# Optimization experiments

Measured on AMD Instinct MI355X. Metric: run time of the kernel, lower is better.

## Reference

```python
import jax, jax.numpy as jnp
import numpy as np

P_DROP = 0.2
NEG_SLOPE = 0.2


def setup_inputs() -> dict:
    key = jax.random.key(0)
    ks = jax.random.split(key, 12)
    N, E = 50000, 800000
    IN, H1, H2, OUT = 256, 256, 128, 64
    x = jax.random.normal(ks[0], (N, IN), dtype=jnp.float32)
    adj_rows = jax.random.randint(ks[1], (E,), 0, N, dtype=jnp.int32)
    adj_cols = jax.random.randint(ks[2], (E,), 0, N, dtype=jnp.int32)
    adj_vals = jax.random.uniform(ks[3], (E,), dtype=jnp.float32)
    W1 = jax.random.normal(ks[4], (H1, IN), dtype=jnp.float32) * (1.0 / np.sqrt(IN))
    b1 = jax.random.normal(ks[5], (H1,), dtype=jnp.float32) * 0.01
    W2 = jax.random.normal(ks[6], (H2, H1), dtype=jnp.float32) * (1.0 / np.sqrt(H1))
    b2 = jax.random.normal(ks[7], (H2,), dtype=jnp.float32) * 0.01
    W3 = jax.random.normal(ks[8], (OUT, H2), dtype=jnp.float32) * (1.0 / np.sqrt(H2))
    b3 = jax.random.normal(ks[9], (OUT,), dtype=jnp.float32) * 0.01
    mask1 = jax.random.bernoulli(ks[10], 1.0 - P_DROP, (N, H1))
    mask2 = jax.random.bernoulli(ks[11], 1.0 - P_DROP, (N, H2))
    return {"x": x, "adj_rows": adj_rows, "adj_cols": adj_cols, "adj_vals": adj_vals,
            "W1": W1, "b1": b1, "W2": W2, "b2": b2, "W3": W3, "b3": b3,
            "mask1": mask1, "mask2": mask2}


def _spmm(rows, cols, vals, h, n_nodes):
    # sparse adjacency matmul: out[r] = sum_e vals[e] * h[cols[e]] for rows[e]==r
    msgs = vals[:, None] * h[cols]  # [E, d] irregular gather
    return jax.ops.segment_sum(msgs, rows, num_segments=n_nodes)


def _gcn_layer(x, W, b, rows, cols, vals, n_nodes):
    h = x @ W.T + b  # nn.Linear
    return _spmm(rows, cols, vals, h, n_nodes)


def reference(x, adj_rows, adj_cols, adj_vals, W1, b1, W2, b2, W3, b3, mask1, mask2):
    N = x.shape[0]
    keep = 1.0 / (1.0 - P_DROP)
    h = _gcn_layer(x, W1, b1, adj_rows, adj_cols, adj_vals, N)
    h = jnp.where(h >= 0, h, NEG_SLOPE * h)
    h = jnp.where(mask1, h * keep, 0.0)
    h = _gcn_layer(h, W2, b2, adj_rows, adj_cols, adj_vals, N)
    h = jnp.where(h >= 0, h, NEG_SLOPE * h)
    h = jnp.where(mask2, h * keep, 0.0)
    z = _gcn_layer(h, W3, b3, adj_rows, adj_cols, adj_vals, N)
    return z
```

## Files before the change

### kernel.cpp

```cpp
#include <hip/hip_runtime.h>


typedef unsigned short ushort_t;
typedef __attribute__((ext_vector_type(8))) short bf16x8;
typedef __attribute__((ext_vector_type(4))) float f32x4;
typedef __attribute__((ext_vector_type(2))) unsigned int u32x2;
typedef __attribute__((ext_vector_type(4))) unsigned int u32x4;

__device__ __forceinline__ float bf2f(ushort_t u) {
  return __uint_as_float(((unsigned int)u) << 16);
}
__device__ __forceinline__ ushort_t f2bf(float f) {
  unsigned int u = __float_as_uint(f);
  return (ushort_t)((u + 0x7FFFu + ((u >> 16) & 1u)) >> 16);
}
__device__ __forceinline__ float read_f(const void* p, int fm, size_t i) {
  return fm ? bf2f(((const ushort_t*)p)[i]) : ((const float*)p)[i];
}

__device__ __forceinline__ size_t frag_off(int m, int k, int K) {
  return (size_t)(m >> 4) * 16 * K + ((size_t)(k >> 5) << 9) +
         (((k >> 3) & 3) << 7) + ((m & 15) << 3) + (k & 7);
}

__device__ __forceinline__ bool mask_keep(const void* mask, int mm, size_t o) {
  switch (mm) {
    case 1:  return ((const int*)mask)[o] != 0;
    case 2:  return ((const unsigned int*)mask)[o] != 0u;
    case 3:  return ((const ushort_t*)mask)[o] != 0;
    default: return ((const unsigned char*)mask)[o] != 0;
  }
}

__global__ void prep_kernel(const void* __restrict__ x,
                            const void* __restrict__ m1,
                            const void* __restrict__ m2,
                            int* __restrict__ modes,
                            int* __restrict__ zero_region, int zn) {
  if (blockIdx.x == 0) {
    __shared__ int bfok;
    if (threadIdx.x == 0) bfok = 1;
    __syncthreads();
    for (int i = threadIdx.x; i < 8192; i += blockDim.x) {
      ushort_t h = ((const ushort_t*)x)[i];
      int e = (h >> 7) & 0xFF;
      if (!(h == 0 || (e >= 95 && e <= 133))) atomicAnd(&bfok, 0);
    }
    __syncthreads();
    if (threadIdx.x == 0) modes[0] = bfok;
  } else if (blockIdx.x <= 2) {
    const void* p = (blockIdx.x == 1) ? m1 : m2;
    __shared__ int ok[4];
    if (threadIdx.x < 4) ok[threadIdx.x] = 1;
    __syncthreads();
    for (int i = threadIdx.x; i < 4096; i += blockDim.x) {
      unsigned int w = ((const unsigned int*)p)[i];
      if (!(w == 0u || w == 1u)) atomicAnd(&ok[0], 0);
      if (!(w == 0u || w == 0x3F800000u)) atomicAnd(&ok[1], 0);
      unsigned int h16 = w >> 16, l16 = w & 0xFFFFu;
      if (!((h16 == 0u || h16 == 0x3F80u) && (l16 == 0u || l16 == 0x3F80u)))
        atomicAnd(&ok[2], 0);
      if (((w | (w >> 8) | (w >> 16) | (w >> 24)) & 0xFEu) != 0u) atomicAnd(&ok[3], 0);
    }
    __syncthreads();
    if (threadIdx.x == 0)
      modes[blockIdx.x] = ok[0] ? 1 : (ok[1] ? 2 : (ok[2] ? 3 : 0));
  } else {
    int i = (blockIdx.x - 3) * blockDim.x + threadIdx.x;
    int stride = (gridDim.x - 3) * blockDim.x;
    for (; i < zn; i += stride) zero_region[i] = 0;
  }
}

__global__ void hist_kernel(const int* __restrict__ rows, int* __restrict__ cnt, int E) {
  int i = blockIdx.x * blockDim.x + threadIdx.x;
  int stride = gridDim.x * blockDim.x;
  for (; i < E; i += stride) atomicAdd(&cnt[rows[i]], 1);
}

__global__ void scan_part_kernel(const int* __restrict__ cnt, int* __restrict__ part, int n) {
  __shared__ int s[256];
  int i = blockIdx.x * 256 + threadIdx.x;
  s[threadIdx.x] = (i < n) ? cnt[i] : 0;
  __syncthreads();
  for (int off = 128; off > 0; off >>= 1) {
    if (threadIdx.x < off) s[threadIdx.x] += s[threadIdx.x + off];
    __syncthreads();
  }
  if (threadIdx.x == 0) part[blockIdx.x] = s[0];
}

__global__ __launch_bounds__(1024) void scan_top_kernel(int* __restrict__ part, int P) {
  __shared__ int s[1024];
  int t = threadIdx.x;
  int v = (t < P) ? part[t] : 0;
  s[t] = v;
  __syncthreads();
  for (int off = 1; off < 1024; off <<= 1) {
    int x = s[t];
    int y = (t >= off) ? s[t - off] : 0;
    __syncthreads();
    s[t] = x + y;
    __syncthreads();
  }
  if (t < P) part[t] = s[t] - v;
}

__global__ void scan_apply_kernel(const int* __restrict__ cnt, const int* __restrict__ part,
                                  int* __restrict__ row_start, int n) {
  __shared__ int s[256];
  int base = part[blockIdx.x];
  int i = blockIdx.x * 256 + threadIdx.x;
  int v = (i < n) ? cnt[i] : 0;
  s[threadIdx.x] = v;
  __syncthreads();
  for (int off = 1; off < 256; off <<= 1) {
    int x = s[threadIdx.x];
    int y = (threadIdx.x >= off) ? s[threadIdx.x - off] : 0;
    __syncthreads();
    s[threadIdx.x] = x + y;
    __syncthreads();
  }
  if (i < n) row_start[i] = base + s[threadIdx.x] - v;
  if (i == n - 1) row_start[n] = base + s[threadIdx.x];
}

__global__ void scatter_convert_kernel(
    const int* __restrict__ rows, const int* __restrict__ cols,
    const void* __restrict__ vals, const int* __restrict__ fm_p,
    const int* __restrict__ row_start, int* __restrict__ fill,
    int* __restrict__ binfill, int2* __restrict__ bins, int cap, int use_bins,
    int2* __restrict__ ecv, int E,
    const void* __restrict__ W1, const void* __restrict__ W2, const void* __restrict__ W3,
    const void* __restrict__ b1, const void* __restrict__ b2, const void* __restrict__ b3,
    const void* __restrict__ x,
    ushort_t* __restrict__ whi, ushort_t* __restrict__ wlo,
    float* __restrict__ biasf, ushort_t* __restrict__ xbf,
    int n1, int n2, int n3, int h1, int h2, int h3, int K1, int K2, int K3,
    int nx) {
  int fm = *fm_p;
  const int BIN_BLOCKS = 512;
  if (blockIdx.x < BIN_BLOCKS) {
    if (use_bins) {
      __shared__ int hist[8];
      __shared__ int gbase[8];
      int tid = threadIdx.x;
      int xcd = blockIdx.x & 7;
      for (int tb = blockIdx.x; tb * 1024 < E; tb += BIN_BLOCKS) {
        int base = tb * 1024;
        if (tid < 8) hist[tid] = 0;
        __syncthreads();
        int rr[4], cc[4], pp[4], rk[4]; float vv[4];
#pragma unroll
        for (int j = 0; j < 4; ++j) {
          int i = base + j * 256 + tid;
          if (i < E) {
            rr[j] = rows[i]; cc[j] = cols[i]; vv[j] = read_f(vals, fm, i);
            pp[j] = rr[j] >> 13;
            rk[j] = atomicAdd(&hist[pp[j]], 1);
          } else {
            pp[j] = -1;
          }
        }
        __syncthreads();
        if (tid < 8)
          gbase[tid] = atomicAdd(&binfill[(xcd << 4) + tid], hist[tid]);
        __syncthreads();
#pragma unroll
        for (int j = 0; j < 4; ++j) {
          if (pp[j] >= 0) {
            int pos = gbase[pp[j]] + rk[j];
            if (pos < cap) {
              bins[(size_t)((xcd << 3) + pp[j]) * cap + pos] =
                  make_int2((rr[j] << 16) | cc[j], __float_as_int(vv[j]));
            } else {
              int pr = atomicAdd(&fill[rr[j]], 1);
              ecv[row_start[rr[j]] + pr] = make_int2(cc[j], __float_as_int(vv[j]));
            }
          }
        }
      }
    } else {
      int i = blockIdx.x * blockDim.x + threadIdx.x;
      int stride = BIN_BLOCKS * blockDim.x;
      for (; i < E; i += stride) {
        int r = rows[i];
        int pos = atomicAdd(&fill[r], 1);
        ecv[row_start[r] + pos] = make_int2(cols[i], __float_as_int(read_f(vals, fm, i)));
      }
    }
  } else {
    int wtot = n1 + n2 + n3;
    int btot = h1 + h2 + h3;
    int nx4 = (fm == 1) ? 0 : nx / 4;
    int total = wtot + btot + nx4;
    int i = (blockIdx.x - BIN_BLOCKS) * blockDim.x + threadIdx.x;
    int stride = (gridDim.x - BIN_BLOCKS) * blockDim.x;
    for (; i < total; i += stride) {
      if (i < wtot) {
        const void* src; int j, K; size_t base;
        if (i < n1) { src = W1; j = i; K = K1; base = 0; }
        else if (i < n1 + n2) { src = W2; j = i - n1; K = K2; base = n1; }
        else { src = W3; j = i - n1 - n2; K = K3; base = (size_t)n1 + n2; }
        int n = j / K, k = j - n * K;
        float v = read_f(src, fm, j);
        ushort_t h = f2bf(v);
        size_t o = base + frag_off(n, k, K);
        whi[o] = h;
        wlo[o] = f2bf(v - bf2f(h));
      } else if (i < wtot + btot) {
        int k = i - wtot;
        const void* src; int j;
        if (k < h1) { src = b1; j = k; }
        else if (k < h1 + h2) { src = b2; j = k - h1; }
        else { src = b3; j = k - h1 - h2; }
        biasf[k] = read_f(src, fm, j);
      } else {
        int k4 = i - wtot - btot;
        int m = k4 / (K1 / 4);
        int k0 = (k4 - m * (K1 / 4)) * 4;
        f32x4 v = ((const f32x4*)x)[k4];
        ushort_t p0 = f2bf(v[0]), p1 = f2bf(v[1]), p2 = f2bf(v[2]), p3 = f2bf(v[3]);
        size_t o = frag_off(m, k0, K1);
        *(u32x2*)(xbf + o) = (u32x2){
            (unsigned int)p0 | ((unsigned int)p1 << 16),
            (unsigned int)p2 | ((unsigned int)p3 << 16)};
      }
    }
  }
}

__global__ __launch_bounds__(256) void bin_scatter_kernel(
    const int2* __restrict__ bins, const int* __restrict__ binfill,
    const int* __restrict__ row_start, int* __restrict__ fill,
    int2* __restrict__ ecv, int cap) {
  int p = blockIdx.x & 7, q = blockIdx.x >> 3;
#pragma unroll 1
  for (int x = 0; x < 8; ++x) {
    int n = binfill[x * 16 + p];
    if (n > cap) n = cap;
    const int2* bp = bins + (size_t)((x << 3) + p) * cap;
    for (int e = q * 256 + (int)threadIdx.x; e < n; e += 128 * 256) {
      int2 ent = bp[e];
      int r = ((unsigned int)ent.x) >> 16;
      int c = ent.x & 0xFFFF;
      int pos = atomicAdd(&fill[r], 1);
      ecv[row_start[r] + pos] = make_int2(c, ent.y);
    }
  }
}

template<int KC>
__device__ __forceinline__ void load_afrag(const ushort_t* __restrict__ A,
                                           const ushort_t* __restrict__ Xrow,
                                           bool rowA, int mtile, int K,
                                           int lane, int mr, int quad, int M,
                                           bf16x8* dst) {
  if (rowA) {
    int rr = mtile * 16 + mr;
    if (rr >= M) rr = M - 1;
    const ushort_t* ap = Xrow + (size_t)rr * K + quad * 8;
#pragma unroll
    for (int kc = 0; kc < KC; ++kc) dst[kc] = *(const bf16x8*)(ap + kc * 32);
  } else {
    const ushort_t* ap = A + (size_t)mtile * 16 * K + lane * 8;
#pragma unroll
    for (int kc = 0; kc < KC; ++kc) dst[kc] = *(const bf16x8*)(ap + kc * 512);
  }
}

template<int KC>
__global__ __launch_bounds__(256) void gemm_breg_kernel(
    const ushort_t* __restrict__ A,
    const ushort_t* __restrict__ Xrow, const int* __restrict__ fm_p,
    const ushort_t* __restrict__ Whi, const ushort_t* __restrict__ Wlo,
    const float* __restrict__ bias, ushort_t* __restrict__ g, int ldg,
    int M, int nct) {
  const int K = KC * 32;
  int wave = threadIdx.x >> 6, lane = threadIdx.x & 63;
  int gw = blockIdx.x * 4 + wave;
  int NW = gridDim.x * 4;
  int mr = lane & 15, quad = lane >> 4;
  int ct = gw % nct;
  int nrt = (M + 15) >> 4;
  int ntasks = nct * nrt;
  if (gw >= ntasks) return;

  bool rowA = (Xrow != nullptr) && (*fm_p != 0);

  bf16x8 wh[KC], wl[KC];
  {
    const ushort_t* wp = Whi + (size_t)ct * 16 * K + lane * 8;
    const ushort_t* wq = Wlo + (size_t)ct * 16 * K + lane * 8;
#pragma unroll
    for (int kc = 0; kc < KC; ++kc) {
      wh[kc] = *(const bf16x8*)(wp + kc * 512);
      wl[kc] = *(const bf16x8*)(wq + kc * 512);
    }
  }
  int col = ct * 16 + mr;
  float bv = bias[col];

  int task = gw;
  bf16x8 af[KC];
  load_afrag<KC>(A, Xrow, rowA, task / nct, K, lane, mr, quad, M, af);

#pragma unroll 1
  for (;;) {
    int next = task + NW;
    bool has_next = next < ntasks;
    bf16x8 afn[KC];
    if (has_next)
      load_afrag<KC>(A, Xrow, rowA, next / nct, K, lane, mr, quad, M, afn);

    f32x4 acc[4];
#pragma unroll
    for (int t = 0; t < 4; ++t) acc[t] = (f32x4){0.f, 0.f, 0.f, 0.f};
#pragma unroll
    for (int kc = 0; kc < KC; ++kc) {
      acc[(2 * kc) & 3] = __builtin_amdgcn_mfma_f32_16x16x32_bf16(af[kc], wh[kc], acc[(2 * kc) & 3], 0, 0, 0);
      acc[(2 * kc + 1) & 3] = __builtin_amdgcn_mfma_f32_16x16x32_bf16(af[kc], wl[kc], acc[(2 * kc + 1) & 3], 0, 0, 0);
    }
    int m0 = (task / nct) * 16;
#pragma unroll
    for (int r = 0; r < 4; ++r) {
      int row = m0 + quad * 4 + r;
      float s = ((acc[0][r] + acc[1][r]) + (acc[2][r] + acc[3][r])) + bv;
      if (row < M) g[(size_t)row * ldg + col] = f2bf(s);
    }
    if (!has_next) break;
#pragma unroll
    for (int kc = 0; kc < KC; ++kc) af[kc] = afn[kc];
    task = next;
  }
}

template<int MODE, int VEC>
__global__ __launch_bounds__(256) void spmm8_kernel(
    const int* __restrict__ row_start, const int2* __restrict__ ecv,
    const ushort_t* __restrict__ G, int D,
    const void* __restrict__ mask, const int* __restrict__ mmode_p,
    void* __restrict__ outp, int N) {
  __shared__ ushort_t stage[1024];
  int wave = threadIdx.x >> 6, lane = threadIdx.x & 63;
  int r = blockIdx.x * 4 + wave;
  bool active = r < N;
  float a[VEC];
#pragma unroll
  for (int q = 0; q < VEC; ++q) a[q] = 0.f;
  int f0 = lane * VEC;

  if (active) {
    int e  = __builtin_amdgcn_readfirstlane(row_start[r]);
    int e1 = __builtin_amdgcn_readfirstlane(row_start[r + 1]);
    for (; e + 8 <= e1; e += 8) {
      int2 cv[8];
#pragma unroll
      for (int j = 0; j < 8; ++j) cv[j] = ecv[e + j];
      if (VEC == 4) {
        u32x2 gg[8];
#pragma unroll
        for (int j = 0; j < 8; ++j)
          gg[j] = *(const u32x2*)(G + (size_t)cv[j].x * D + f0);
#pragma unroll
        for (int j = 0; j < 8; ++j) {
          float v = __int_as_float(cv[j].y);
          a[0] += v * bf2f((ushort_t)gg[j][0]);
          a[1] += v * bf2f((ushort_t)(gg[j][0] >> 16));
          a[2] += v * bf2f((ushort_t)gg[j][1]);
          a[3] += v * bf2f((ushort_t)(gg[j][1] >> 16));
        }
      } else if (VEC == 2) {
        unsigned int gg[8];
#pragma unroll
        for (int j = 0; j < 8; ++j)
          gg[j] = *(const unsigned int*)(G + (size_t)cv[j].x * D + f0);
#pragma unroll
        for (int j = 0; j < 8; ++j) {
          float v = __int_as_float(cv[j].y);
          a[0] += v * bf2f((ushort_t)gg[j]);
          a[1] += v * bf2f((ushort_t)(gg[j] >> 16));
        }
      } else {
        ushort_t h[8];
#pragma unroll
        for (int j = 0; j < 8; ++j) h[j] = G[(size_t)cv[j].x * D + f0];
#pragma unroll
        for (int j = 0; j < 8; ++j) a[0] += __int_as_float(cv[j].y) * bf2f(h[j]);
      }
    }
    if (e < e1) {
      int idx[8]; float v[8];
#pragma unroll
      for (int j = 0; j < 8; ++j) {
        int ee = e + j;
        bool ok = ee < e1;
        int2 cv = ecv[ok ? ee : e1 - 1];
        idx[j] = cv.x;
        v[j] = ok ? __int_as_float(cv.y) : 0.f;
      }
      if (VEC == 4) {
        u32x2 gg[8];
#pragma unroll
        for (int j = 0; j < 8; ++j)
          gg[j] = *(const u32x2*)(G + (size_t)idx[j] * D + f0);
#pragma unroll
        for (int j = 0; j < 8; ++j) {
          a[0] += v[j] * bf2f((ushort_t)gg[j][0]);
          a[1] += v[j] * bf2f((ushort_t)(gg[j][0] >> 16));
          a[2] += v[j] * bf2f((ushort_t)gg[j][1]);
          a[3] += v[j] * bf2f((ushort_t)(gg[j][1] >> 16));
        }
      } else if (VEC == 2) {
        unsigned int gg[8];
#pragma unroll
        for (int j = 0; j < 8; ++j)
          gg[j] = *(const unsigned int*)(G + (size_t)idx[j] * D + f0);
#pragma unroll
        for (int j = 0; j < 8; ++j) {
          a[0] += v[j] * bf2f((ushort_t)gg[j]);
          a[1] += v[j] * bf2f((ushort_t)(gg[j] >> 16));
        }
      } else {
        ushort_t h[8];
#pragma unroll
        for (int j = 0; j < 8; ++j) h[j] = G[(size_t)idx[j] * D + f0];
#pragma unroll
        for (int j = 0; j < 8; ++j) a[0] += v[j] * bf2f(h[j]);
      }
    }
  }

  if (MODE == 1) {
    if (active) {
      size_t om = (size_t)r * D + f0;
      int mm = *mmode_p;
      bool keep[VEC];
      if (mm == 1 || mm == 2) {
        if (VEC == 4) {
          u32x4 mv = *(const u32x4*)((const unsigned int*)mask + om);
#pragma unroll
          for (int q = 0; q < VEC; ++q) keep[q] = mv[q] != 0u;
        } else if (VEC == 2) {
          u32x2 mv = *(const u32x2*)((const unsigned int*)mask + om);
#pragma unroll
          for (int q = 0; q < VEC; ++q) keep[q] = mv[q] != 0u;
        } else {
          keep[0] = ((const unsigned int*)mask)[om] != 0u;
        }
      } else if (mm == 3) {
        if (VEC == 4) {
          u32x2 mv = *(const u32x2*)((const ushort_t*)mask + om);
          keep[0] = (mv[0] & 0xFFFFu) != 0u; keep[1] = (mv[0] >> 16) != 0u;
          keep[2] = (mv[1] & 0xFFFFu) != 0u; keep[3] = (mv[1] >> 16) != 0u;
        } else if (VEC == 2) {
          unsigned int mv = *(const unsigned int*)((const ushort_t*)mask + om);
          keep[0] = (mv & 0xFFFFu) != 0u; keep[1] = (mv >> 16) != 0u;
        } else {
          keep[0] = ((const ushort_t*)mask)[om] != 0;
        }
      } else {
        if (VEC == 4) {
          unsigned int mv = *(const unsigned int*)((const unsigned char*)mask + om);
          keep[0] = (mv & 0xFFu) != 0u;        keep[1] = ((mv >> 8) & 0xFFu) != 0u;
          keep[2] = ((mv >> 16) & 0xFFu) != 0u; keep[3] = (mv >> 24) != 0u;
        } else if (VEC == 2) {
          unsigned int mv = *(const unsigned short*)((const unsigned char*)mask + om);
          keep[0] = (mv & 0xFFu) != 0u; keep[1] = ((mv >> 8) & 0xFFu) != 0u;
        } else {
          keep[0] = ((const unsigned char*)mask)[om] != 0;
        }
      }
#pragma unroll
      for (int q = 0; q < VEC; ++q) {
        float t = a[q];
        t = (t >= 0.f) ? t : 0.2f * t;
        t = keep[q] ? t * 1.25f : 0.f;
        stage[wave * D + f0 + q] = f2bf(t);
      }
    }
    __syncthreads();
    if (threadIdx.x < D) {
      int g = threadIdx.x >> 3, s = threadIdx.x & 7;
      int kc = g >> 2, quad = g & 3;
      int sr = s >> 1;
      int r0 = blockIdx.x * 4;
      if (r0 + sr < N) {
        int kk = kc * 32 + quad * 8 + (s & 1) * 4;
        size_t dst = (size_t)(r0 >> 4) * 16 * D + ((size_t)kc << 9) +
                     (quad << 7) + ((r0 & 15) << 3) + s * 4;
        *(u32x2*)((ushort_t*)outp + dst) = *(const u32x2*)(stage + sr * D + kk);
      }
    }
  } else {
    if (active) {
      size_t o = (size_t)r * D + f0;
#pragma unroll
      for (int q = 0; q < VEC; ++q) ((float*)outp)[o + q] = a[q];
    }
  }
}

extern "C" void kernel_launch(void* const* d_in, const int* in_sizes, int n_in,
                              void* d_out, int out_size, void* d_ws, size_t ws_size,
                              hipStream_t stream) {
  const void* x     = d_in[0];
  const int*  rows  = (const int*)d_in[1];
  const int*  cols  = (const int*)d_in[2];
  const void* vals  = d_in[3];
  const void* W1    = d_in[4];
  const void* b1    = d_in[5];
  const void* W2    = d_in[6];
  const void* b2    = d_in[7];
  const void* W3    = d_in[8];
  const void* b3    = d_in[9];
  const void* mask1 = d_in[10];
  const void* mask2 = d_in[11];

  const int H1  = in_sizes[5];
  const int H2  = in_sizes[7];
  const int OUT = in_sizes[9];
  const int IN  = in_sizes[4] / H1;
  const int N   = in_sizes[0] / IN;
  const int E   = in_sizes[1];
  const int W1n = in_sizes[4], W2n = in_sizes[6], W3n = in_sizes[8];
  const int Np  = ((N + 15) / 16) * 16;
  const int CAP = (E >> 5) + 2048;
  const int use_bins = (N <= 65535) ? 1 : 0;

  char* ws = (char*)d_ws;
  size_t off = 0;
  auto alloc = [&](size_t bytes) -> void* {
    void* p = ws + off;
    off = (off + bytes + 255) & ~(size_t)255;
    return p;
  };
  int*      modes     = (int*)alloc(4 * 4);
  int*      row_start = (int*)alloc((size_t)(N + 1) * 4);
  int*      cnt       = (int*)alloc((size_t)N * 8 + 512);
  int*      part      = (int*)alloc(1024 * 4);
  int2*     ecv       = (int2*)alloc((size_t)E * 8);
  int2*     bins      = (int2*)alloc((size_t)64 * CAP * 8);
  ushort_t* whi       = (ushort_t*)alloc((size_t)(W1n + W2n + W3n) * 2);
  ushort_t* wlo       = (ushort_t*)alloc((size_t)(W1n + W2n + W3n) * 2);
  float*    biasf     = (float*)alloc((size_t)(H1 + H2 + OUT) * 4);
  ushort_t* bufA      = (ushort_t*)alloc((size_t)Np * H1 * 2);
  ushort_t* bufB      = (ushort_t*)alloc((size_t)Np * H1 * 2);
  ushort_t* bufC      = (ushort_t*)alloc((size_t)Np * H1 * 2);

  int* fmode   = modes;
  int* mm1     = modes + 1;
  int* mm2     = modes + 2;
  int* fill    = cnt + N;
  int* binfill = cnt + 2 * N;
  ushort_t* w1hi = whi,             *w1lo = wlo;
  ushort_t* w2hi = whi + W1n,       *w2lo = wlo + W1n;
  ushort_t* w3hi = whi + W1n + W2n, *w3lo = wlo + W1n + W2n;

  prep_kernel<<<259, 256, 0, stream>>>(x, mask1, mask2, modes, cnt, 2 * N + 128);

  const int P = (N + 255) / 256;
  hist_kernel<<<1024, 256, 0, stream>>>(rows, cnt, E);
  scan_part_kernel<<<P, 256, 0, stream>>>(cnt, part, N);
  scan_top_kernel<<<1, 1024, 0, stream>>>(part, P);
  scan_apply_kernel<<<P, 256, 0, stream>>>(cnt, part, row_start, N);

  scatter_convert_kernel<<<2560, 256, 0, stream>>>(
      rows, cols, vals, fmode, row_start, fill, binfill, bins, CAP, use_bins,
      ecv, E, W1, W2, W3, b1, b2, b3, x, whi, wlo, biasf, bufA,
      W1n, W2n, W3n, H1, H2, OUT, IN, H1, H2, N * IN);
  if (use_bins) {
    bin_scatter_kernel<<<1024, 256, 0, stream>>>(
        bins, binfill, row_start, fill, ecv, CAP);
  }

  const int GEMM_BLOCKS = 1024;
  int spmm_grid = (N + 3) / 4;

  gemm_breg_kernel<8><<<GEMM_BLOCKS, 256, 0, stream>>>(
      bufA, (const ushort_t*)x, fmode, w1hi, w1lo, biasf, bufB, H1, N, H1 / 16);
  spmm8_kernel<1, 4><<<spmm_grid, 256, 0, stream>>>(
      row_start, ecv, bufB, H1, mask1, mm1, bufC, N);
  gemm_breg_kernel<8><<<GEMM_BLOCKS, 256, 0, stream>>>(
      bufC, nullptr, fmode, w2hi, w2lo, biasf + H1, bufB, H2, N, H2 / 16);
  spmm8_kernel<1, 2><<<spmm_grid, 256, 0, stream>>>(
      row_start, ecv, bufB, H2, mask2, mm2, bufA, N);
  gemm_breg_kernel<4><<<GEMM_BLOCKS, 256, 0, stream>>>(
      bufA, nullptr, fmode, w3hi, w3lo, biasf + H1 + H2, bufB, OUT, N, OUT / 16);
  spmm8_kernel<0, 1><<<spmm_grid, 256, 0, stream>>>(
      row_start, ecv, bufB, OUT, nullptr, fmode, d_out, N);
}
```

Baseline: 441.7 us.

## Restructure CSR build: fuse histogram into binning, overlap scatter with first GEMM

Weight and bias conversion moves into the prep kernel. The row histogram is fused into the binning pass, whose overflow entries now go to a separate buffer instead of being written to CSR directly. The final CSR scatter shares one launch with the layer-1 GEMM, which does not depend on the CSR. This removes two launches and a separate pass over the rows array, and lets the atomic-heavy scatter run alongside GEMM work. The cost is extra atomics on cnt inside the binning loop, a serialised overflow counter, and an extra E-sized workspace buffer.

Result: faster. 423.9 us (-4.0%).

```diff
diff --git a/kernel.cpp b/kernel.cpp
--- a/kernel.cpp
+++ b/kernel.cpp
@@ -23,20 +23,19 @@
          (((k >> 3) & 3) << 7) + ((m & 15) << 3) + (k & 7);
 }
 
-__device__ __forceinline__ bool mask_keep(const void* mask, int mm, size_t o) {
-  switch (mm) {
-    case 1:  return ((const int*)mask)[o] != 0;
-    case 2:  return ((const unsigned int*)mask)[o] != 0u;
-    case 3:  return ((const ushort_t*)mask)[o] != 0;
-    default: return ((const unsigned char*)mask)[o] != 0;
-  }
-}
-
 __global__ void prep_kernel(const void* __restrict__ x,
                             const void* __restrict__ m1,
                             const void* __restrict__ m2,
                             int* __restrict__ modes,
-                            int* __restrict__ zero_region, int zn) {
+                            int* __restrict__ zero_region, int zn,
+                            const void* __restrict__ W1, const void* __restrict__ W2,
+                            const void* __restrict__ W3,
+                            const void* __restrict__ b1, const void* __restrict__ b2,
+                            const void* __restrict__ b3,
+                            ushort_t* __restrict__ whi, ushort_t* __restrict__ wlo,
+                            float* __restrict__ biasf,
+                            int n1, int n2, int n3, int h1, int h2, int h3,
+                            int K1, int K2, int K3) {
   if (blockIdx.x == 0) {
     __shared__ int bfok;
     if (threadIdx.x == 0) bfok = 1;
@@ -65,17 +64,45 @@
     __syncthreads();
     if (threadIdx.x == 0)
       modes[blockIdx.x] = ok[0] ? 1 : (ok[1] ? 2 : (ok[2] ? 3 : 0));
+  } else if (blockIdx.x < 35) {
+    __shared__ int bfok;
+    if (threadIdx.x == 0) bfok = 1;
+    __syncthreads();
+    for (int i = threadIdx.x; i < 8192; i += blockDim.x) {
+      ushort_t h = ((const ushort_t*)x)[i];
+      int e = (h >> 7) & 0xFF;
+      if (!(h == 0 || (e >= 95 && e <= 133))) atomicAnd(&bfok, 0);
+    }
+    __syncthreads();
+    int fm = bfok;
+    int wtot = n1 + n2 + n3;
+    int total = wtot + h1 + h2 + h3;
+    for (int i = (blockIdx.x - 3) * 256 + threadIdx.x; i < total; i += 32 * 256) {
+      if (i < wtot) {
+        const void* src; int j, K; size_t base;
+        if (i < n1) { src = W1; j = i; K = K1; base = 0; }
+        else if (i < n1 + n2) { src = W2; j = i - n1; K = K2; base = n1; }
+        else { src = W3; j = i - n1 - n2; K = K3; base = (size_t)n1 + n2; }
+        int n = j / K, k = j - n * K;
+        float v = read_f(src, fm, j);
+        ushort_t h = f2bf(v);
+        size_t o = base + frag_off(n, k, K);
+        whi[o] = h;
+        wlo[o] = f2bf(v - bf2f(h));
+      } else {
+        int k = i - wtot;
+        const void* src; int j;
+        if (k < h1) { src = b1; j = k; }
+        else if (k < h1 + h2) { src = b2; j = k - h1; }
+        else { src = b3; j = k - h1 - h2; }
+        biasf[k] = read_f(src, fm, j);
+      }
+    }
   } else {
-    int i = (blockIdx.x - 3) * blockDim.x + threadIdx.x;
-    int stride = (gridDim.x - 3) * blockDim.x;
+    int i = (blockIdx.x - 35) * blockDim.x + threadIdx.x;
+    int stride = (gridDim.x - 35) * blockDim.x;
     for (; i < zn; i += stride) zero_region[i] = 0;
   }
-}
-
-__global__ void hist_kernel(const int* __restrict__ rows, int* __restrict__ cnt, int E) {
-  int i = blockIdx.x * blockDim.x + threadIdx.x;
-  int stride = gridDim.x * blockDim.x;
-  for (; i < E; i += stride) atomicAdd(&cnt[rows[i]], 1);
 }
 
 __global__ void scan_part_kernel(const int* __restrict__ cnt, int* __restrict__ part, int n) {
@@ -125,19 +152,13 @@
   if (i == n - 1) row_start[n] = base + s[threadIdx.x];
 }
 
-__global__ void scatter_convert_kernel(
+__global__ void hist_bin_kernel(
     const int* __restrict__ rows, const int* __restrict__ cols,
     const void* __restrict__ vals, const int* __restrict__ fm_p,
-    const int* __restrict__ row_start, int* __restrict__ fill,
-    int* __restrict__ binfill, int2* __restrict__ bins, int cap, int use_bins,
-    int2* __restrict__ ecv, int E,
-    const void* __restrict__ W1, const void* __restrict__ W2, const void* __restrict__ W3,
-    const void* __restrict__ b1, const void* __restrict__ b2, const void* __restrict__ b3,
-    const void* __restrict__ x,
-    ushort_t* __restrict__ whi, ushort_t* __restrict__ wlo,
-    float* __restrict__ biasf, ushort_t* __restrict__ xbf,
-    int n1, int n2, int n3, int h1, int h2, int h3, int K1, int K2, int K3,
-    int nx) {
+    int* __restrict__ cnt, int* __restrict__ binfill,
+    int2* __restrict__ bins, int cap, int use_bins, int2* __restrict__ ovf,
+    int E, const void* __restrict__ x, ushort_t* __restrict__ xbf,
+    int K1, int nx) {
   int fm = *fm_p;
   const int BIN_BLOCKS = 512;
   if (blockIdx.x < BIN_BLOCKS) {
@@ -156,6 +177,7 @@
           int i = base + j * 256 + tid;
           if (i < E) {
             rr[j] = rows[i]; cc[j] = cols[i]; vv[j] = read_f(vals, fm, i);
+            atomicAdd(&cnt[rr[j]], 1);
             pp[j] = rr[j] >> 13;
             rk[j] = atomicAdd(&hist[pp[j]], 1);
           } else {
@@ -174,8 +196,8 @@
               bins[(size_t)((xcd << 3) + pp[j]) * cap + pos] =
                   make_int2((rr[j] << 16) | cc[j], __float_as_int(vv[j]));
             } else {
-              int pr = atomicAdd(&fill[rr[j]], 1);
-              ecv[row_start[rr[j]] + pr] = make_int2(cc[j], __float_as_int(vv[j]));
+              int op = atomicAdd(&binfill[128], 1);
+              ovf[op] = make_int2((rr[j] << 16) | cc[j], __float_as_int(vv[j]));
             }
           }
         }
@@ -183,69 +205,22 @@
     } else {
       int i = blockIdx.x * blockDim.x + threadIdx.x;
       int stride = BIN_BLOCKS * blockDim.x;
-      for (; i < E; i += stride) {
-        int r = rows[i];
-        int pos = atomicAdd(&fill[r], 1);
-        ecv[row_start[r] + pos] = make_int2(cols[i], __float_as_int(read_f(vals, fm, i)));
-      }
+      for (; i < E; i += stride) atomicAdd(&cnt[rows[i]], 1);
     }
   } else {
-    int wtot = n1 + n2 + n3;
-    int btot = h1 + h2 + h3;
-    int nx4 = (fm == 1) ? 0 : nx / 4;
-    int total = wtot + btot + nx4;
+    if (fm == 1) return;
+    int nx4 = nx / 4;
     int i = (blockIdx.x - BIN_BLOCKS) * blockDim.x + threadIdx.x;
     int stride = (gridDim.x - BIN_BLOCKS) * blockDim.x;
-    for (; i < total; i += stride) {
-      if (i < wtot) {
-        const void* src; int j, K; size_t base;
-        if (i < n1) { src = W1; j = i; K = K1; base = 0; }
-        else if (i < n1 + n2) { src = W2; j = i - n1; K = K2; base = n1; }
-        else { src = W3; j = i - n1 - n2; K = K3; base = (size_t)n1 + n2; }
-        int n = j / K, k = j - n * K;
-        float v = read_f(src, fm, j);
-        ushort_t h = f2bf(v);
-        size_t o = base + frag_off(n, k, K);
-        whi[o] = h;
-        wlo[o] = f2bf(v - bf2f(h));
-      } else if (i < wtot + btot) {
-        int k = i - wtot;
-        const void* src; int j;
-        if (k < h1) { src = b1; j = k; }
-        else if (k < h1 + h2) { src = b2; j = k - h1; }
-        else { src = b3; j = k - h1 - h2; }
-        biasf[k] = read_f(src, fm, j);
-      } else {
-        int k4 = i - wtot - btot;
-        int m = k4 / (K1 / 4);
-        int k0 = (k4 - m * (K1 / 4)) * 4;
-        f32x4 v = ((const f32x4*)x)[k4];
-        ushort_t p0 = f2bf(v[0]), p1 = f2bf(v[1]), p2 = f2bf(v[2]), p3 = f2bf(v[3]);
-        size_t o = frag_off(m, k0, K1);
-        *(u32x2*)(xbf + o) = (u32x2){
-            (unsigned int)p0 | ((unsigned int)p1 << 16),
-            (unsigned int)p2 | ((unsigned int)p3 << 16)};
-      }
-    }
-  }
-}
-
-__global__ __launch_bounds__(256) void bin_scatter_kernel(
-    const int2* __restrict__ bins, const int* __restrict__ binfill,
-    const int* __restrict__ row_start, int* __restrict__ fill,
-    int2* __restrict__ ecv, int cap) {
-  int p = blockIdx.x & 7, q = blockIdx.x >> 3;
-#pragma unroll 1
-  for (int x = 0; x < 8; ++x) {
-    int n = binfill[x * 16 + p];
-    if (n > cap) n = cap;
-    const int2* bp = bins + (size_t)((x << 3) + p) * cap;
-    for (int e = q * 256 + (int)threadIdx.x; e < n; e += 128 * 256) {
-      int2 ent = bp[e];
-      int r = ((unsigned int)ent.x) >> 16;
-      int c = ent.x & 0xFFFF;
-      int pos = atomicAdd(&fill[r], 1);
-      ecv[row_start[r] + pos] = make_int2(c, ent.y);
+    for (; i < nx4; i += stride) {
+      int m = i / (K1 / 4);
+      int k0 = (i - m * (K1 / 4)) * 4;
+      f32x4 v = ((const f32x4*)x)[i];
+      ushort_t p0 = f2bf(v[0]), p1 = f2bf(v[1]), p2 = f2bf(v[2]), p3 = f2bf(v[3]);
+      size_t o = frag_off(m, k0, K1);
+      *(u32x2*)(xbf + o) = (u32x2){
+          (unsigned int)p0 | ((unsigned int)p1 << 16),
+          (unsigned int)p2 | ((unsigned int)p3 << 16)};
     }
   }
 }
@@ -270,23 +245,23 @@
 }
 
 template<int KC>
-__global__ __launch_bounds__(256) void gemm_breg_kernel(
-    const ushort_t* __restrict__ A,
-    const ushort_t* __restrict__ Xrow, const int* __restrict__ fm_p,
+__device__ __forceinline__ void gemm_dev(
+    int vbid, int nblk, int tid,
+    const ushort_t* __restrict__ A, const ushort_t* __restrict__ Xrow, int fm,
     const ushort_t* __restrict__ Whi, const ushort_t* __restrict__ Wlo,
     const float* __restrict__ bias, ushort_t* __restrict__ g, int ldg,
     int M, int nct) {
   const int K = KC * 32;
-  int wave = threadIdx.x >> 6, lane = threadIdx.x & 63;
-  int gw = blockIdx.x * 4 + wave;
-  int NW = gridDim.x * 4;
+  int wave = tid >> 6, lane = tid & 63;
+  int gw = vbid * 4 + wave;
+  int NW = nblk * 4;
   int mr = lane & 15, quad = lane >> 4;
   int ct = gw % nct;
   int nrt = (M + 15) >> 4;
   int ntasks = nct * nrt;
   if (gw >= ntasks) return;
 
-  bool rowA = (Xrow != nullptr) && (*fm_p != 0);
+  bool rowA = (Xrow != nullptr) && (fm != 0);
 
   bf16x8 wh[KC], wl[KC];
   {
@@ -332,6 +307,66 @@
 #pragma unroll
     for (int kc = 0; kc < KC; ++kc) af[kc] = afn[kc];
     task = next;
+  }
+}
+
+template<int KC>
+__global__ __launch_bounds__(256) void gemm_breg_kernel(
+    const ushort_t* __restrict__ A,
+    const ushort_t* __restrict__ Xrow, const int* __restrict__ fm_p,
+    const ushort_t* __restrict__ Whi, const ushort_t* __restrict__ Wlo,
+    const float* __restrict__ bias, ushort_t* __restrict__ g, int ldg,
+    int M, int nct) {
+  gemm_dev<KC>(blockIdx.x, gridDim.x, threadIdx.x, A, Xrow, *fm_p,
+               Whi, Wlo, bias, g, ldg, M, nct);
+}
+
+__global__ __launch_bounds__(256) void scatter_gemm_kernel(
+    const int2* __restrict__ bins, const int* __restrict__ binfill,
+    const int* __restrict__ row_start, int* __restrict__ fill,
+    int2* __restrict__ ecv, int cap, const int2* __restrict__ ovf,
+    const int* __restrict__ rows, const int* __restrict__ cols,
+    const void* __restrict__ vals, const int* __restrict__ fm_p,
+    int use_bins, int E,
+    const ushort_t* __restrict__ A, const ushort_t* __restrict__ Xrow,
+    const ushort_t* __restrict__ Whi, const ushort_t* __restrict__ Wlo,
+    const float* __restrict__ bias, ushort_t* __restrict__ g, int ldg,
+    int M, int nct) {
+  if (blockIdx.x >= 1024) {
+    gemm_dev<8>(blockIdx.x - 1024, 1024, threadIdx.x, A, Xrow, *fm_p,
+                Whi, Wlo, bias, g, ldg, M, nct);
+    return;
+  }
+  if (use_bins) {
+    int p = blockIdx.x & 7, q = blockIdx.x >> 3;
+#pragma unroll 1
+    for (int x = 0; x < 8; ++x) {
+      int n = binfill[x * 16 + p];
+      if (n > cap) n = cap;
+      const int2* bp = bins + (size_t)((x << 3) + p) * cap;
+      for (int e = q * 256 + (int)threadIdx.x; e < n; e += 128 * 256) {
+        int2 ent = bp[e];
+        int r = ((unsigned int)ent.x) >> 16;
+        int c = ent.x & 0xFFFF;
+        int pos = atomicAdd(&fill[r], 1);
+        ecv[row_start[r] + pos] = make_int2(c, ent.y);
+      }
+    }
+    int ovfn = binfill[128];
+    for (int e = blockIdx.x * 256 + (int)threadIdx.x; e < ovfn; e += 1024 * 256) {
+      int2 ent = ovf[e];
+      int r = ((unsigned int)ent.x) >> 16;
+      int c = ent.x & 0xFFFF;
+      int pos = atomicAdd(&fill[r], 1);
+      ecv[row_start[r] + pos] = make_int2(c, ent.y);
+    }
+  } else {
+    int fm = *fm_p;
+    for (int i = blockIdx.x * 256 + (int)threadIdx.x; i < E; i += 1024 * 256) {
+      int r = rows[i];
+      int pos = atomicAdd(&fill[r], 1);
+      ecv[row_start[r] + pos] = make_int2(cols[i], __float_as_int(read_f(vals, fm, i)));
+    }
   }
 }
 
@@ -537,10 +572,11 @@
   };
   int*      modes     = (int*)alloc(4 * 4);
   int*      row_start = (int*)alloc((size_t)(N + 1) * 4);
-  int*      cnt       = (int*)alloc((size_t)N * 8 + 512);
+  int*      cnt       = (int*)alloc((size_t)N * 8 + 768);
   int*      part      = (int*)alloc(1024 * 4);
   int2*     ecv       = (int2*)alloc((size_t)E * 8);
   int2*     bins      = (int2*)alloc((size_t)64 * CAP * 8);
+  int2*     ovf       = (int2*)alloc((size_t)E * 8);
   ushort_t* whi       = (ushort_t*)alloc((size_t)(W1n + W2n + W3n) * 2);
   ushort_t* wlo       = (ushort_t*)alloc((size_t)(W1n + W2n + W3n) * 2);
   float*    biasf     = (float*)alloc((size_t)(H1 + H2 + OUT) * 4);
@@ -557,28 +593,28 @@
   ushort_t* w2hi = whi + W1n,       *w2lo = wlo + W1n;
   ushort_t* w3hi = whi + W1n + W2n, *w3lo = wlo + W1n + W2n;
 
-  prep_kernel<<<259, 256, 0, stream>>>(x, mask1, mask2, modes, cnt, 2 * N + 128);
+  prep_kernel<<<512, 256, 0, stream>>>(
+      x, mask1, mask2, modes, cnt, 2 * N + 132,
+      W1, W2, W3, b1, b2, b3, whi, wlo, biasf,
+      W1n, W2n, W3n, H1, H2, OUT, IN, H1, H2);
+
+  hist_bin_kernel<<<1536, 256, 0, stream>>>(
+      rows, cols, vals, fmode, cnt, binfill, bins, CAP, use_bins, ovf,
+      E, x, bufA, IN, N * IN);
 
   const int P = (N + 255) / 256;
-  hist_kernel<<<1024, 256, 0, stream>>>(rows, cnt, E);
   scan_part_kernel<<<P, 256, 0, stream>>>(cnt, part, N);
   scan_top_kernel<<<1, 1024, 0, stream>>>(part, P);
   scan_apply_kernel<<<P, 256, 0, stream>>>(cnt, part, row_start, N);
 
-  scatter_convert_kernel<<<2560, 256, 0, stream>>>(
-      rows, cols, vals, fmode, row_start, fill, binfill, bins, CAP, use_bins,
-      ecv, E, W1, W2, W3, b1, b2, b3, x, whi, wlo, biasf, bufA,
-      W1n, W2n, W3n, H1, H2, OUT, IN, H1, H2, N * IN);
-  if (use_bins) {
-    bin_scatter_kernel<<<1024, 256, 0, stream>>>(
-        bins, binfill, row_start, fill, ecv, CAP);
-  }
-
+  scatter_gemm_kernel<<<2048, 256, 0, stream>>>(
+      bins, binfill, row_start, fill, ecv, CAP, ovf,
+      rows, cols, vals, fmode, use_bins, E,
+      bufA, (const ushort_t*)x, w1hi, w1lo, biasf, bufB, H1, N, H1 / 16);
+
+  int spmm_grid = (N + 3) / 4;
   const int GEMM_BLOCKS = 1024;
-  int spmm_grid = (N + 3) / 4;
-
-  gemm_breg_kernel<8><<<GEMM_BLOCKS, 256, 0, stream>>>(
-      bufA, (const ushort_t*)x, fmode, w1hi, w1lo, biasf, bufB, H1, N, H1 / 16);
+
   spmm8_kernel<1, 4><<<spmm_grid, 256, 0, stream>>>(
       row_start, ecv, bufB, H1, mask1, mm1, bufC, N);
   gemm_breg_kernel<8><<<GEMM_BLOCKS, 256, 0, stream>>>(
```
